# Optimization experiments

Hardware: AMD Instinct MI355X
Metric: run time of the kernel (lower is better)

Reference implementation:

```python
import jax, jax.numpy as jnp
import numpy as np

EPS = 1e-5

def setup_inputs() -> dict:
    key = jax.random.key(0)
    ks = jax.random.split(key, 7)
    C = 512
    x = jax.random.normal(ks[0], (16, C, 32, 32), dtype=jnp.float32)
    gn_w = jax.random.normal(ks[1], (C,), dtype=jnp.float32) * 0.02 + 1.0
    gn_b = jax.random.normal(ks[2], (C,), dtype=jnp.float32) * 0.02
    qkv_w = jax.random.normal(ks[3], (3 * C, C), dtype=jnp.float32) * (1.0 / np.sqrt(C))
    qkv_b = jax.random.normal(ks[4], (3 * C,), dtype=jnp.float32) * 0.02
    proj_w = jax.random.normal(ks[5], (C, C), dtype=jnp.float32) * (1.0 / np.sqrt(C))
    proj_b = jax.random.normal(ks[6], (C,), dtype=jnp.float32) * 0.02
    return {"x": x, "gn_w": gn_w, "gn_b": gn_b, "qkv_w": qkv_w,
            "qkv_b": qkv_b, "proj_w": proj_w, "proj_b": proj_b}

def reference(x, gn_w, gn_b, qkv_w, qkv_b, proj_w, proj_b):
    B, C, H, W = x.shape
    S = H * W
    # GroupNorm with 1 group: normalize over (C,H,W) per sample
    mean = jnp.mean(x, axis=(1, 2, 3), keepdims=True)
    var = jnp.var(x, axis=(1, 2, 3), keepdims=True)
    h = (x - mean) * jax.lax.rsqrt(var + EPS)
    h = h * gn_w[None, :, None, None] + gn_b[None, :, None, None]
    # 1x1 conv qkv: [B,C,H,W] -> [B,3C,H,W], flatten spatial -> [B,S,3C]
    hf = h.reshape(B, C, S)  # b c s
    qkv = jnp.einsum('bcs,oc->bso', hf, qkv_w) + qkv_b  # [B,S,3C]
    q, k, v = jnp.split(qkv, 3, axis=-1)  # each [B,S,C]
    scale = C ** (-0.5)
    attn = jax.nn.softmax(jnp.einsum('bqc,bkc->bqk', q, k) * scale, axis=-1)
    out = jnp.einsum('bqk,bkc->bqc', attn, v)  # [B,S,C]
    out = jnp.einsum('bsc,oc->bso', out, proj_w) + proj_b
    out = out.transpose(0, 2, 1).reshape(B, C, H, W)
    return x + out
```

## Files before the change

kernel.cpp:

```cpp
#include <hip/hip_runtime.h>
#include <stdint.h>

#define B_  16
#define C_  512
#define S_  1024
#define NSAMP (C_*S_)

typedef __bf16 bf16x8 __attribute__((ext_vector_type(8)));
typedef float  f32x4  __attribute__((ext_vector_type(4)));

__device__ __forceinline__ float bf2f(uint16_t u){ return __uint_as_float(((uint32_t)u)<<16); }
__device__ __forceinline__ uint16_t f2bf(float f){
  uint32_t u = __float_as_uint(f);
  uint32_t r = u + 0x7fffu + ((u>>16)&1u);
  return (uint16_t)(r>>16);
}
__device__ __forceinline__ float wsum(float v){
  #pragma unroll
  for(int o=32;o;o>>=1) v += __shfl_xor(v,o,64);
  return v;
}
__device__ __forceinline__ int wsumi(int v){
  #pragma unroll
  for(int o=32;o;o>>=1) v += __shfl_xor(v,o,64);
  return v;
}
__device__ __forceinline__ void gload16(const void* g, void* l){
  __builtin_amdgcn_global_load_lds(
      (__attribute__((address_space(1))) void*)g,
      (__attribute__((address_space(3))) void*)l, 16, 0, 0);
}

__device__ __forceinline__ void convseg(const void* src, uint16_t* dst, int n, int f, int t){
  const int idx = t*8;
  if (idx >= n) return;
  if (f){
    const float* s = (const float*)src;
    float4 v0 = *(const float4*)(s + idx);
    float4 v1 = *(const float4*)(s + idx + 4);
    ushort4 a, b;
    a.x=f2bf(v0.x); a.y=f2bf(v0.y); a.z=f2bf(v0.z); a.w=f2bf(v0.w);
    b.x=f2bf(v1.x); b.y=f2bf(v1.y); b.z=f2bf(v1.z); b.w=f2bf(v1.w);
    *(ushort4*)(dst + idx)     = a;
    *(ushort4*)(dst + idx + 4) = b;
  } else {
    *(uint4*)(dst + idx) = *(const uint4*)((const uint16_t*)src + idx);
  }
}
__global__ __launch_bounds__(256) void prep_k(
    const void* __restrict__ srcx, uint16_t* __restrict__ xb, float2* __restrict__ part,
    const void* qkvw, const void* projw, const void* gnw, const void* gnb,
    const void* qkvb, const void* projb,
    uint16_t* qkvwb, uint16_t* projwb, uint16_t* gnwb, uint16_t* gnbb,
    uint16_t* qkvbb, uint16_t* projbb, int* __restrict__ flag){
  const int t = threadIdx.x;
  __shared__ int sdet[4];
  int f;
  {
    const uint4 v = ((const uint4*)srcx)[t & 255];
    uint32_t ww[4] = {v.x, v.y, v.z, v.w};
    int c = 0;
    #pragma unroll
    for(int q=0;q<4;q++) c += ((((ww[q] & 0xffffu) >> 7) & 0xffu) >= 132) ? 1 : 0;
    c = wsumi(c);
    if ((t & 63) == 0) sdet[t >> 6] = c;
    __syncthreads();
    f = (sdet[0] + sdet[1] + sdet[2] + sdet[3] > 128) ? 1 : 0;
  }
  if (blockIdx.x == 0 && t == 0) *flag = f;

  if (blockIdx.x >= 1024){
    const int bid = blockIdx.x - 1024;
    if (bid < 384){
      const size_t off = (size_t)bid*2048;
      convseg((const char*)qkvw + off*(f?4:2), qkvwb + off, 2048, f, t);
    } else if (bid < 512){
      const size_t off = (size_t)(bid-384)*2048;
      convseg((const char*)projw + off*(f?4:2), projwb + off, 2048, f, t);
    } else {
      convseg(gnw,   gnwb,   512,  f, t);
      convseg(gnb,   gnbb,   512,  f, t);
      convseg(qkvb,  qkvbb,  1536, f, t);
      convseg(projb, projbb, 512,  f, t);
    }
    return;
  }
  const size_t base = (size_t)blockIdx.x * 8192;
  float s = 0.f, s2 = 0.f;
  if (f){
    const float4* sp = (const float4*)((const float*)srcx + base);
    ushort4* dp = (ushort4*)(xb + base);
    #pragma unroll
    for(int i=0;i<8;i++){
      float4 v = sp[i*256 + t];
      s  += v.x + v.y + v.z + v.w;
      s2 += v.x*v.x + v.y*v.y + v.z*v.z + v.w*v.w;
      ushort4 o; o.x=f2bf(v.x); o.y=f2bf(v.y); o.z=f2bf(v.z); o.w=f2bf(v.w);
      dp[i*256 + t] = o;
    }
  } else {
    const uint4* sp = (const uint4*)((const uint16_t*)srcx + base);
    uint4* dp = (uint4*)(xb + base);
    #pragma unroll
    for(int i=0;i<4;i++){
      uint4 p = sp[i*256 + t];
      dp[i*256 + t] = p;
      uint32_t uu[4] = {p.x,p.y,p.z,p.w};
      #pragma unroll
      for(int q=0;q<4;q++){
        float f0 = __uint_as_float(uu[q]<<16);
        float f1 = __uint_as_float(uu[q] & 0xffff0000u);
        s += f0 + f1; s2 += f0*f0 + f1*f1;
      }
    }
  }
  s = wsum(s); s2 = wsum(s2);
  __shared__ float rs[4], rq[4];
  const int lane = t & 63, w = t >> 6;
  if (lane==0){ rs[w]=s; rq[w]=s2; }
  __syncthreads();
  if (t==0)
    part[blockIdx.x] = make_float2(rs[0]+rs[1]+rs[2]+rs[3], rq[0]+rq[1]+rq[2]+rq[3]);
}

__global__ __launch_bounds__(256) void gn_apply_t(const uint16_t* __restrict__ x,
    const uint16_t* __restrict__ gw, const uint16_t* __restrict__ gb,
    const float2* __restrict__ part, uint16_t* __restrict__ hT){
  __shared__ float tile[64*129];
  const int b = blockIdx.z, c0 = blockIdx.y<<6, s0 = blockIdx.x<<7;
  const int t = threadIdx.x;
  float2 p = part[b*64 + (t & 63)];
  float s = wsum(p.x), s2 = wsum(p.y);
  const float ninv = 1.f/(float)NSAMP;
  const float mn = s*ninv;
  const float rstd = rsqrtf(s2*ninv - mn*mn + 1e-5f);
  #pragma unroll
  for(int k=0;k<4;k++){
    const int ci = t + k*256;
    const int cl = ci>>4, sc = ci&15;
    uint4 v = *(const uint4*)&x[((size_t)b*C_ + c0+cl)*S_ + s0 + sc*8];
    const uint16_t* e = (const uint16_t*)&v;
    float* dst = &tile[cl*129 + sc*8];
    #pragma unroll
    for(int q=0;q<8;q++) dst[q] = bf2f(e[q]);
  }
  __syncthreads();
  const int cc = t & 7;
  const int sb0 = t >> 3;
  uint4 wv4 = *(const uint4*)&gw[c0 + cc*8];
  uint4 bv4 = *(const uint4*)&gb[c0 + cc*8];
  const uint16_t* we = (const uint16_t*)&wv4;
  const uint16_t* be = (const uint16_t*)&bv4;
  float aq[8], cq[8];
  #pragma unroll
  for(int q=0;q<8;q++){ aq[q] = bf2f(we[q])*rstd; cq[q] = bf2f(be[q]) - mn*aq[q]; }
  #pragma unroll
  for(int k=0;k<4;k++){
    const int sl = sb0 + k*32;
    uint16_t ov[8];
    #pragma unroll
    for(int q=0;q<8;q++){
      float xv = tile[(cc*8+q)*129 + sl];
      ov[q] = f2bf(xv*aq[q] + cq[q]);
    }
    uint4 o;
    o.x = (uint32_t)ov[0] | ((uint32_t)ov[1]<<16);
    o.y = (uint32_t)ov[2] | ((uint32_t)ov[3]<<16);
    o.z = (uint32_t)ov[4] | ((uint32_t)ov[5]<<16);
    o.w = (uint32_t)ov[6] | ((uint32_t)ov[7]<<16);
    *(uint4*)&hT[((size_t)b*S_ + s0+sl)*C_ + c0 + cc*8] = o;
  }
}

__global__ __launch_bounds__(256)
void qkv_k(const uint16_t* __restrict__ hT, const uint16_t* __restrict__ qkvw,
           const uint16_t* __restrict__ qkvb, uint16_t* __restrict__ qk,
           uint16_t* __restrict__ Vt)
{
  __shared__ uint16_t smem[16384];
  uint16_t* As = smem;
  uint16_t* Bs = smem + 8192;
  const int tid = threadIdx.x;
  const int lane = tid & 63, w = tid >> 6;
  const int quad = lane >> 4, lm = lane & 15;
  const int wm = (w & 1) << 6, wn = (w >> 1) << 6;

  const bool vpath = blockIdx.x >= 1024;
  const int id = vpath ? (blockIdx.x - 1024) : blockIdx.x;
  const int r8 = id & 7, k8 = id >> 3;
  int m0, n0, bz;
  const uint16_t *Abase, *Bbase;
  if (!vpath){
    const int g = r8*16 + (k8 & 15);
    m0 = g << 7; n0 = (k8 >> 4) << 7; bz = 0;
    Abase = hT + (size_t)m0*512;
    Bbase = qkvw + (size_t)n0*512;
  } else {
    const int g = r8*16 + (k8 & 15);
    m0 = (k8 >> 4) << 7; n0 = (g & 7) << 7; bz = g >> 3;
    Abase = qkvw + (size_t)(1024 + m0)*512;
    Bbase = hT + (size_t)bz*S_*C_ + (size_t)n0*512;
  }

  f32x4 acc[4][4];
  #pragma unroll
  for(int i=0;i<4;i++)
    #pragma unroll
    for(int j=0;j<4;j++) acc[i][j] = (f32x4){0.f,0.f,0.f,0.f};

  const int srow = tid >> 3;
  const int sx   = (tid & 7) ^ (srow & 7);
  const uint16_t* ga = Abase + (size_t)srow*512 + sx*8;
  const uint16_t* gb = Bbase + (size_t)srow*512 + sx*8;
  uint16_t* sa = &As[tid*8];
  uint16_t* sb = &Bs[tid*8];

  for(int k0=0;k0<512;k0+=64){
    #pragma unroll
    for(int i=0;i<4;i++){
      gload16(ga + (size_t)(i*32)*512 + k0, sa + i*2048);
      gload16(gb + (size_t)(i*32)*512 + k0, sb + i*2048);
    }
    __syncthreads();
    #pragma unroll
    for(int kk=0;kk<64;kk+=32){
      bf16x8 av[4], bv[4];
      #pragma unroll
      for(int i=0;i<4;i++){
        const int row = wm + i*16 + lm;
        av[i] = *(const bf16x8*)&As[row*64 + ((((kk>>3)+quad) ^ (row&7))<<3)];
      }
      #pragma unroll
      for(int j=0;j<4;j++){
        const int row = wn + j*16 + lm;
        bv[j] = *(const bf16x8*)&Bs[row*64 + ((((kk>>3)+quad) ^ (row&7))<<3)];
      }
      #pragma unroll
      for(int i=0;i<4;i++)
        #pragma unroll
        for(int j=0;j<4;j++)
          acc[i][j] = __builtin_amdgcn_mfma_f32_16x16x32_bf16(av[i], bv[j], acc[i][j], 0,0,0);
    }
    __syncthreads();
  }

  uint16_t* Cs = smem;
  if (!vpath){
    #pragma unroll
    for(int j=0;j<4;j++){
      const int col_l = wn + j*16 + lm;
      const float bvv = bf2f(qkvb[n0 + col_l]);
      #pragma unroll
      for(int i=0;i<4;i++){
        const int rl0 = wm + i*16 + (quad<<2);
        #pragma unroll
        for(int r=0;r<4;r++)
          Cs[(rl0+r)*128 + col_l] = f2bf(acc[i][j][r] + bvv);
      }
    }
  } else {
    #pragma unroll
    for(int i=0;i<4;i++){
      const int rl0 = wm + i*16 + (quad<<2);
      #pragma unroll
      for(int r=0;r<4;r++){
        const float bvv = bf2f(qkvb[1024 + m0 + rl0 + r]);
        #pragma unroll
        for(int j=0;j<4;j++)
          Cs[(rl0+r)*128 + wn + j*16 + lm] = f2bf(acc[i][j][r] + bvv);
      }
    }
  }
  __syncthreads();
  uint16_t* base = vpath ? (Vt + (size_t)bz*C_*S_) : qk;
  #pragma unroll
  for(int k=0;k<8;k++){
    const int ci = tid + k*256;
    const int rl = ci>>4, ccc = ci&15;
    *(uint4*)&base[(size_t)(m0+rl)*1024 + n0 + ccc*8] = *(const uint4*)&Cs[rl*128 + ccc*8];
  }
}

template<bool HASBIAS, bool BIASROW, bool OUTDYN, bool HASRES, int SWZMODE, bool EXP, int RSMODE>
__global__ __launch_bounds__(256)
void gemm_bt(const uint16_t* __restrict__ A, const uint16_t* __restrict__ Bt,
             void* __restrict__ Cp, const uint16_t* __restrict__ bias,
             const uint16_t* __restrict__ xres, const int* __restrict__ flag,
             float* __restrict__ rs_part,
             int lda, int ldb, int ldc, int K,
             long long sA, long long sB, long long sC)
{
  __shared__ uint16_t smem[16384];
  uint16_t* As = smem;
  uint16_t* Bs = smem + 8192;
  const int lin = (blockIdx.z * gridDim.y + blockIdx.y) * gridDim.x + blockIdx.x;
  const int r8 = lin & 7, kk8 = lin >> 3;
  int bx, by, bz;
  if (SWZMODE == 0){
    const int G = (gridDim.y * gridDim.z) >> 3;
    const int g = r8 * G + (kk8 % G);
    bx = kk8 / G; by = g % gridDim.y; bz = g / gridDim.y;
  } else {
    const int G = (gridDim.x * gridDim.z) >> 3;
    const int g = r8 * G + (kk8 % G);
    by = kk8 / G; bx = g % gridDim.x; bz = g / gridDim.x;
  }

  const int tid = threadIdx.x;
  const int lane = tid & 63, w = tid >> 6;
  const int quad = lane >> 4, lm = lane & 15;
  const int m0 = by << 7, n0 = bx << 7;
  A  += (size_t)bz * sA;
  Bt += (size_t)bz * sB;

  f32x4 acc[4][4];
  #pragma unroll
  for(int i=0;i<4;i++)
    #pragma unroll
    for(int j=0;j<4;j++) acc[i][j] = (f32x4){0.f,0.f,0.f,0.f};

  const int wm = (w & 1) << 6, wn = (w >> 1) << 6;
  const int srow = tid >> 3;
  const int sx   = (tid & 7) ^ (srow & 7);
  const uint16_t* ga = A  + (size_t)(m0 + srow)*lda + sx*8;
  const uint16_t* gb = Bt + (size_t)(n0 + srow)*ldb + sx*8;
  uint16_t* sa = &As[tid*8];
  uint16_t* sb = &Bs[tid*8];

  for(int k0=0;k0<K;k0+=64){
    #pragma unroll
    for(int i=0;i<4;i++){
      gload16(ga + (size_t)(i*32)*lda + k0, sa + i*2048);
      gload16(gb + (size_t)(i*32)*ldb + k0, sb + i*2048);
    }
    __syncthreads();
    #pragma unroll
    for(int kk=0;kk<64;kk+=32){
      bf16x8 av[4], bv[4];
      #pragma unroll
      for(int i=0;i<4;i++){
        const int row = wm + i*16 + lm;
        av[i] = *(const bf16x8*)&As[row*64 + ((((kk>>3)+quad) ^ (row&7))<<3)];
      }
      #pragma unroll
      for(int j=0;j<4;j++){
        const int row = wn + j*16 + lm;
        bv[j] = *(const bf16x8*)&Bs[row*64 + ((((kk>>3)+quad) ^ (row&7))<<3)];
      }
      #pragma unroll
      for(int i=0;i<4;i++)
        #pragma unroll
        for(int j=0;j<4;j++)
          acc[i][j] = __builtin_amdgcn_mfma_f32_16x16x32_bf16(av[i], bv[j], acc[i][j], 0,0,0);
    }
    __syncthreads();
  }

  const size_t cb = (size_t)bz * (size_t)sC;
  if (!OUTDYN && !HASRES){
    uint16_t* Cs = smem;
    float rp[4][4];
    if (RSMODE == 1){
      #pragma unroll
      for(int i=0;i<4;i++)
        #pragma unroll
        for(int r=0;r<4;r++) rp[i][r] = 0.f;
    }
    float inv[4][4];
    if (RSMODE == 2){
      const int myrow = m0 + wm + lm*4 + quad;
      const float4* rpp = (const float4*)&rs_part[((size_t)bz*1024 + myrow)*16];
      float4 a0 = rpp[0], a1 = rpp[1], a2 = rpp[2], a3 = rpp[3];
      float rowsumv = a0.x+a0.y+a0.z+a0.w + a1.x+a1.y+a1.z+a1.w
                    + a2.x+a2.y+a2.z+a2.w + a3.x+a3.y+a3.z+a3.w;
      #pragma unroll
      for(int i=0;i<4;i++)
        #pragma unroll
        for(int r=0;r<4;r++)
          inv[i][r] = 1.f / __shfl(rowsumv, r*16 + i*4 + quad, 64);
    }
    #pragma unroll
    for(int j=0;j<4;j++){
      const int col_l = wn + j*16 + lm;
      const float cbias = (HASBIAS && !BIASROW) ? bf2f(bias[n0 + col_l]) : 0.f;
      #pragma unroll
      for(int i=0;i<4;i++){
        const int rl0 = wm + i*16 + (quad<<2);
        #pragma unroll
        for(int r=0;r<4;r++){
          float v = acc[i][j][r] + cbias;
          if (HASBIAS && BIASROW) v += bf2f(bias[m0 + rl0 + r]);
          if (EXP)          v = __expf(v * 0.044194173824159216f);
          if (RSMODE == 1)  rp[i][r] += v;
          if (RSMODE == 2)  v *= inv[i][r];
          Cs[(rl0+r)*128 + col_l] = f2bf(v);
        }
      }
    }
    if (RSMODE == 1){
      #pragma unroll
      for(int i=0;i<4;i++)
        #pragma unroll
        for(int r=0;r<4;r++){
          float s4 = rp[i][r];
          #pragma unroll
          for(int o=8;o;o>>=1) s4 += __shfl_xor(s4, o, 64);
          if (lm == 0)
            rs_part[((size_t)bz*1024 + m0 + wm + i*16 + (quad<<2) + r)*16 + (bx<<1) + (w>>1)] = s4;
        }
    }
    __syncthreads();
    uint16_t* base = (uint16_t*)Cp + cb;
    #pragma unroll
    for(int k=0;k<8;k++){
      const int ci = tid + k*256;
      const int rl = ci>>4, cc = ci&15;
      *(uint4*)&base[(size_t)(m0+rl)*ldc + n0 + cc*8] = *(const uint4*)&Cs[rl*128 + cc*8];
    }
  } else {
    float* Cs32 = (float*)smem;
    const int f = OUTDYN ? *flag : 0;
    const int wnh = wn >> 1;
    #pragma unroll
    for(int half=0; half<2; ++half){
      #pragma unroll
      for(int j2=0;j2<2;j2++){
        const int j = half*2 + j2;
        const int col_l = wn + j*16 + lm;
        const int hcol = wnh + j2*16 + lm;
        const float cbias = (HASBIAS && !BIASROW) ? bf2f(bias[n0 + col_l]) : 0.f;
        #pragma unroll
        for(int i=0;i<4;i++){
          const int rl0 = wm + i*16 + (quad<<2);
          #pragma unroll
          for(int r=0;r<4;r++){
            float v = acc[i][j][r] + cbias;
            if (HASBIAS && BIASROW) v += bf2f(bias[m0 + rl0 + r]);
            if (EXP) v = __expf(v * 0.044194173824159216f);
            Cs32[(rl0+r)*64 + hcol] = v;
          }
        }
      }
      __syncthreads();
      #pragma unroll
      for(int k=0;k<8;k++){
        const int ci = tid + k*256;
        const int rl = ci>>4, c4 = ci&15;
        float4 vv = *(const float4*)&Cs32[rl*64 + c4*4];
        const int gcol = n0 + c4*4 + ((c4>=8)?32:0) + half*32;
        const size_t idx = cb + (size_t)(m0+rl)*ldc + gcol;
        float o0=vv.x, o1=vv.y, o2=vv.z, o3=vv.w;
        if (HASRES){
          uint2 rr = *(const uint2*)&xres[idx];
          o0 += bf2f((uint16_t)(rr.x & 0xffffu));
          o1 += bf2f((uint16_t)(rr.x >> 16));
          o2 += bf2f((uint16_t)(rr.y & 0xffffu));
          o3 += bf2f((uint16_t)(rr.y >> 16));
        }
        if (OUTDYN && f){
          float4 o = make_float4(o0,o1,o2,o3);
          *(float4*)&((float*)Cp)[idx] = o;
        } else {
          uint2 o;
          o.x = (uint32_t)f2bf(o0) | ((uint32_t)f2bf(o1)<<16);
          o.y = (uint32_t)f2bf(o2) | ((uint32_t)f2bf(o3)<<16);
          *(uint2*)&((uint16_t*)Cp)[idx] = o;
        }
      }
      __syncthreads();
    }
  }
}

extern "C" void kernel_launch(void* const* d_in, const int* in_sizes, int n_in,
                              void* d_out, int out_size, void* d_ws, size_t ws_size,
                              hipStream_t stream){
  char* ws = (char*)d_ws;
  int*      flag  = (int*)ws;
  float2*   part  = (float2*)(ws + 4096);
  uint16_t* gnwb  = (uint16_t*)(ws + 16384);
  uint16_t* gnbb  = (uint16_t*)(ws + 17408);
  uint16_t* qkvbb = (uint16_t*)(ws + 18432);
  uint16_t* projbb= (uint16_t*)(ws + 21504);
  uint16_t* qkvwb = (uint16_t*)(ws + 32768);
  uint16_t* projwb= (uint16_t*)(ws + 1605632);
  float*    rs_part=(float*)  (ws + 2129920);
  uint16_t* xb    = (uint16_t*)(ws + 4194304);
  uint16_t* hT    = (uint16_t*)(ws + 20971520);
  uint16_t* qk    = (uint16_t*)(ws + 37748736);
  uint16_t* sc    = (uint16_t*)(ws + 71303168);
  uint16_t* Vt    = (uint16_t*)(ws + 104857600);

  hipLaunchKernelGGL(prep_k, dim3(1537), dim3(256), 0, stream,
                     d_in[0], xb, part,
                     d_in[3], d_in[5], d_in[1], d_in[2], d_in[4], d_in[6],
                     qkvwb, projwb, gnwb, gnbb, qkvbb, projbb, flag);
  hipLaunchKernelGGL(gn_apply_t, dim3(8,8,16), dim3(256), 0, stream, xb, gnwb, gnbb, part, hT);

  hipLaunchKernelGGL(qkv_k, dim3(1536), dim3(256), 0, stream, hT, qkvwb, qkvbb, qk, Vt);

  hipLaunchKernelGGL((gemm_bt<false,false,false,false,0,true,1>), dim3(8,8,16), dim3(256), 0, stream,
      qk, qk + 512, (void*)sc, (const uint16_t*)nullptr, (const uint16_t*)nullptr, flag, rs_part,
      1024, 1024, 1024, 512, (long long)S_*1024, (long long)S_*1024, (long long)S_*S_);

  hipLaunchKernelGGL((gemm_bt<false,false,false,false,0,false,2>), dim3(4,8,16), dim3(256), 0, stream,
      sc, Vt, (void*)hT, (const uint16_t*)nullptr, (const uint16_t*)nullptr, flag, rs_part,
      1024, 1024, 512, 1024, (long long)S_*S_, (long long)C_*S_, (long long)S_*C_);

  hipLaunchKernelGGL((gemm_bt<true,true,true,true,1,false,0>), dim3(8,4,16), dim3(256), 0, stream,
      projwb, hT, d_out, projbb, xb, flag, (float*)nullptr,
      512, 512, 1024, 512, 0LL, (long long)S_*C_, (long long)C_*S_);
}
```

Baseline: 216.4 us.

## Double-buffer LDS tiles in qkv and generic GEMM kernels to overlap loads

Both GEMM kernels now use two shared-memory buffers for the A/B tiles. The next K-tile's global-to-LDS loads are issued before computing on the current tile, with explicit vmcnt waits and raw barriers in place of __syncthreads. This is meant to hide global load latency behind MFMA work. The cost is that LDS use per block doubles to 64KB, which may reduce occupancy, and the manual waitcnt logic relies on the exact count of outstanding loads.

```diff
diff --git a/kernel.cpp b/kernel.cpp
--- a/kernel.cpp
+++ b/kernel.cpp
@@ -177,9 +177,7 @@
            const uint16_t* __restrict__ qkvb, uint16_t* __restrict__ qk,
            uint16_t* __restrict__ Vt)
 {
-  __shared__ uint16_t smem[16384];
-  uint16_t* As = smem;
-  uint16_t* Bs = smem + 8192;
+  __shared__ uint16_t smem[32768];
   const int tid = threadIdx.x;
   const int lane = tid & 63, w = tid >> 6;
   const int quad = lane >> 4, lm = lane & 15;
@@ -212,28 +210,45 @@
   const int sx   = (tid & 7) ^ (srow & 7);
   const uint16_t* ga = Abase + (size_t)srow*512 + sx*8;
   const uint16_t* gb = Bbase + (size_t)srow*512 + sx*8;
-  uint16_t* sa = &As[tid*8];
-  uint16_t* sb = &Bs[tid*8];
-
-  for(int k0=0;k0<512;k0+=64){
-    #pragma unroll
-    for(int i=0;i<4;i++){
-      gload16(ga + (size_t)(i*32)*512 + k0, sa + i*2048);
-      gload16(gb + (size_t)(i*32)*512 + k0, sb + i*2048);
-    }
-    __syncthreads();
+  uint16_t* sa0 = &smem[tid*8];
+  uint16_t* sb0 = &smem[8192 + tid*8];
+  uint16_t* sa1 = &smem[16384 + tid*8];
+  uint16_t* sb1 = &smem[24576 + tid*8];
+
+  #pragma unroll
+  for(int i=0;i<4;i++){
+    gload16(ga + (size_t)(i*32)*512, sa0 + i*2048);
+    gload16(gb + (size_t)(i*32)*512, sb0 + i*2048);
+  }
+  for(int t=0;t<8;t++){
+    if (t < 7){
+      uint16_t* na = (t&1) ? sa0 : sa1;
+      uint16_t* nb = (t&1) ? sb0 : sb1;
+      const int k1 = (t+1)<<6;
+      #pragma unroll
+      for(int i=0;i<4;i++){
+        gload16(ga + (size_t)(i*32)*512 + k1, na + i*2048);
+        gload16(gb + (size_t)(i*32)*512 + k1, nb + i*2048);
+      }
+      asm volatile("s_waitcnt vmcnt(8)" ::: "memory");
+    } else {
+      asm volatile("s_waitcnt vmcnt(0)" ::: "memory");
+    }
+    __builtin_amdgcn_s_barrier();
+    __builtin_amdgcn_sched_barrier(0);
+    const int boff = (t&1) << 14;
     #pragma unroll
     for(int kk=0;kk<64;kk+=32){
       bf16x8 av[4], bv[4];
       #pragma unroll
       for(int i=0;i<4;i++){
         const int row = wm + i*16 + lm;
-        av[i] = *(const bf16x8*)&As[row*64 + ((((kk>>3)+quad) ^ (row&7))<<3)];
+        av[i] = *(const bf16x8*)&smem[boff + row*64 + ((((kk>>3)+quad) ^ (row&7))<<3)];
       }
       #pragma unroll
       for(int j=0;j<4;j++){
         const int row = wn + j*16 + lm;
-        bv[j] = *(const bf16x8*)&Bs[row*64 + ((((kk>>3)+quad) ^ (row&7))<<3)];
+        bv[j] = *(const bf16x8*)&smem[boff + 8192 + row*64 + ((((kk>>3)+quad) ^ (row&7))<<3)];
       }
       #pragma unroll
       for(int i=0;i<4;i++)
@@ -241,7 +256,7 @@
         for(int j=0;j<4;j++)
           acc[i][j] = __builtin_amdgcn_mfma_f32_16x16x32_bf16(av[i], bv[j], acc[i][j], 0,0,0);
     }
-    __syncthreads();
+    __builtin_amdgcn_s_barrier();
   }
 
   uint16_t* Cs = smem;
@@ -290,9 +305,7 @@
              int lda, int ldb, int ldc, int K,
              long long sA, long long sB, long long sC)
 {
-  __shared__ uint16_t smem[16384];
-  uint16_t* As = smem;
-  uint16_t* Bs = smem + 8192;
+  __shared__ uint16_t smem[32768];
   const int lin = (blockIdx.z * gridDim.y + blockIdx.y) * gridDim.x + blockIdx.x;
   const int r8 = lin & 7, kk8 = lin >> 3;
   int bx, by, bz;
@@ -324,28 +337,46 @@
   const int sx   = (tid & 7) ^ (srow & 7);
   const uint16_t* ga = A  + (size_t)(m0 + srow)*lda + sx*8;
   const uint16_t* gb = Bt + (size_t)(n0 + srow)*ldb + sx*8;
-  uint16_t* sa = &As[tid*8];
-  uint16_t* sb = &Bs[tid*8];
-
-  for(int k0=0;k0<K;k0+=64){
-    #pragma unroll
-    for(int i=0;i<4;i++){
-      gload16(ga + (size_t)(i*32)*lda + k0, sa + i*2048);
-      gload16(gb + (size_t)(i*32)*ldb + k0, sb + i*2048);
-    }
-    __syncthreads();
+  uint16_t* sa0 = &smem[tid*8];
+  uint16_t* sb0 = &smem[8192 + tid*8];
+  uint16_t* sa1 = &smem[16384 + tid*8];
+  uint16_t* sb1 = &smem[24576 + tid*8];
+
+  const int NT = K >> 6;
+  #pragma unroll
+  for(int i=0;i<4;i++){
+    gload16(ga + (size_t)(i*32)*lda, sa0 + i*2048);
+    gload16(gb + (size_t)(i*32)*ldb, sb0 + i*2048);
+  }
+  for(int t=0;t<NT;t++){
+    if (t < NT-1){
+      uint16_t* na = (t&1) ? sa0 : sa1;
+      uint16_t* nb = (t&1) ? sb0 : sb1;
+      const int k1 = (t+1)<<6;
+      #pragma unroll
+      for(int i=0;i<4;i++){
+        gload16(ga + (size_t)(i*32)*lda + k1, na + i*2048);
+        gload16(gb + (size_t)(i*32)*ldb + k1, nb + i*2048);
+      }
+      asm volatile("s_waitcnt vmcnt(8)" ::: "memory");
+    } else {
+      asm volatile("s_waitcnt vmcnt(0)" ::: "memory");
+    }
+    __builtin_amdgcn_s_barrier();
+    __builtin_amdgcn_sched_barrier(0);
+    const int boff = (t&1) << 14;
     #pragma unroll
     for(int kk=0;kk<64;kk+=32){
       bf16x8 av[4], bv[4];
       #pragma unroll
       for(int i=0;i<4;i++){
         const int row = wm + i*16 + lm;
-        av[i] = *(const bf16x8*)&As[row*64 + ((((kk>>3)+quad) ^ (row&7))<<3)];
+        av[i] = *(const bf16x8*)&smem[boff + row*64 + ((((kk>>3)+quad) ^ (row&7))<<3)];
       }
       #pragma unroll
       for(int j=0;j<4;j++){
         const int row = wn + j*16 + lm;
-        bv[j] = *(const bf16x8*)&Bs[row*64 + ((((kk>>3)+quad) ^ (row&7))<<3)];
+        bv[j] = *(const bf16x8*)&smem[boff + 8192 + row*64 + ((((kk>>3)+quad) ^ (row&7))<<3)];
       }
       #pragma unroll
       for(int i=0;i<4;i++)
@@ -353,7 +384,7 @@
         for(int j=0;j<4;j++)
           acc[i][j] = __builtin_amdgcn_mfma_f32_16x16x32_bf16(av[i], bv[j], acc[i][j], 0,0,0);
     }
-    __syncthreads();
+    __builtin_amdgcn_s_barrier();
   }
 
   const size_t cb = (size_t)bz * (size_t)sC;
```

Result: faster. 204.3 us (median of 2 runs) (-5.6%).
